# Kernel tuning notes

Measured on AMD Instinct MI355X. Metric: run time of the kernel, lower is better.

The kernel has to match this reference:

```python
import jax, jax.numpy as jnp
import numpy as np

N_TRIALS, T, INPUT_DIM = 32, 512, 64
N, R, OUTPUT_DIM = 4096, 8, 64
DT = 0.1


def setup_inputs() -> dict:
    key = jax.random.key(0)
    k_inp, k_B, k_W, k_m, k_n = jax.random.split(key, 5)
    inp = jax.random.normal(k_inp, (N_TRIALS, T, INPUT_DIM), dtype=jnp.float32)
    B = jax.random.normal(k_B, (N, INPUT_DIM), dtype=jnp.float32)
    W = jax.random.normal(k_W, (OUTPUT_DIM, N), dtype=jnp.float32) / np.sqrt(N)
    m = jax.random.normal(k_m, (N, R), dtype=jnp.float32)
    n = jax.random.normal(k_n, (N, R), dtype=jnp.float32)
    return {"inp": inp, "B": B, "W": W, "m": m, "n": n}


def reference(inp, B, W, m, n):
    # inp: [b, t, i]; B: [N, i]; W: [o, N]; m, n: [N, r]
    n_trials = inp.shape[0]
    # Precompute input projection for all steps: [t, b, N]
    inp_proj = jnp.einsum('bti,ni->tbn', inp, B)

    def step(x, u):
        # x: [b, N] voltage; u: [b, N] projected input at this step
        # sigmoid(x) @ (m n^T / N)^T == ((sigmoid(x) @ n) @ m^T) / N
        rec = (jax.nn.sigmoid(x) @ n) @ m.T / N
        x_new = (1.0 - DT) * x + DT * (rec + u)
        y = jax.nn.sigmoid(x_new) @ W.T  # [b, o]
        return x_new, (x_new, y)

    x0 = jnp.zeros((n_trials, N), dtype=inp.dtype)
    _, (xs, ys) = jax.lax.scan(step, x0, inp_proj)
    # xs: [t, b, N]; ys: [t, b, o]
    x_seq = jnp.concatenate([x0[None], xs], axis=0).transpose(1, 0, 2)  # [b, t+1, N]
    output_seq = ys.transpose(1, 0, 2)  # [b, t, o]
    return (x_seq, output_seq)
```

## Files before the change

### kernel.cpp

```cpp
#include <hip/hip_runtime.h>

static constexpr int BTRIALS = 32;
static constexpr int TSTEPS  = 512;
static constexpr int IDIM    = 64;
static constexpr int NDIM    = 4096;
static constexpr int RDIM    = 8;
static constexpr int ODIM    = 64;

__device__ __forceinline__ float fast_sigmoid(float x) {
    float e = __builtin_amdgcn_exp2f(x * -1.44269504088896340736f);
    return __builtin_amdgcn_rcpf(1.0f + e);
}

template <int CTRL, int RMASK>
__device__ __forceinline__ float dpp_add(float v) {
    int moved = __builtin_amdgcn_update_dpp(0, __float_as_int(v), CTRL, RMASK, 0xf, true);
    return v + __int_as_float(moved);
}

__device__ __forceinline__ float wave_reduce_to_lane63(float v) {
    v = dpp_add<0x111, 0xf>(v);
    v = dpp_add<0x112, 0xf>(v);
    v = dpp_add<0x114, 0xf>(v);
    v = dpp_add<0x118, 0xf>(v);
    v = dpp_add<0x142, 0xa>(v);
    v = dpp_add<0x143, 0xc>(v);
    return v;
}

__device__ __forceinline__ short f2bf(float f) {
    unsigned u = __float_as_uint(f);
    u += 0x7FFFu + ((u >> 16) & 1u);
    return (short)(u >> 16);
}

__global__ __launch_bounds__(256) void pre_gemm(const float* __restrict__ inp,
                                                const float* __restrict__ Bm,
                                                float* __restrict__ u,
                                                int t0, int rows) {
    __shared__ __align__(16) float At[64][68];
    __shared__ __align__(16) float Bt[64][68];
    const int tid = threadIdx.x;
    const int c4  = (tid & 15) * 4;
    const int rq  = tid >> 4;
    const int mbase = blockIdx.x * 64;
    const int nbase = blockIdx.y * 64;

    #pragma unroll
    for (int rr = 0; rr < 4; ++rr) {
        const int rloc = rr * 16 + rq;
        const int mr = mbase + rloc;
        float4 a = make_float4(0.f, 0.f, 0.f, 0.f);
        if (mr < rows) {
            const int b  = mr & 31;
            const int tl = mr >> 5;
            a = *(const float4*)(inp + ((size_t)b * TSTEPS + (t0 + tl)) * IDIM + c4);
        }
        At[c4 + 0][rloc] = a.x; At[c4 + 1][rloc] = a.y;
        At[c4 + 2][rloc] = a.z; At[c4 + 3][rloc] = a.w;
        const int n = nbase + rloc;
        float4 bb = *(const float4*)(Bm + (size_t)n * IDIM + c4);
        Bt[c4 + 0][rloc] = bb.x; Bt[c4 + 1][rloc] = bb.y;
        Bt[c4 + 2][rloc] = bb.z; Bt[c4 + 3][rloc] = bb.w;
    }
    __syncthreads();

    const int m4 = (tid >> 4) * 4;
    const int n4 = (tid & 15) * 4;
    float acc[4][4];
    #pragma unroll
    for (int i = 0; i < 4; ++i)
        #pragma unroll
        for (int j = 0; j < 4; ++j) acc[i][j] = 0.f;

    #pragma unroll 8
    for (int k = 0; k < 64; ++k) {
        float4 a = *(const float4*)&At[k][m4];
        float4 w = *(const float4*)&Bt[k][n4];
        float av[4] = {a.x, a.y, a.z, a.w};
        float wv[4] = {w.x, w.y, w.z, w.w};
        #pragma unroll
        for (int i = 0; i < 4; ++i)
            #pragma unroll
            for (int j = 0; j < 4; ++j)
                acc[i][j] = fmaf(av[i], wv[j], acc[i][j]);
    }

    #pragma unroll
    for (int i = 0; i < 4; ++i) {
        const int mr = mbase + m4 + i;
        if (mr < rows) {
            float4 o = make_float4(acc[i][0] * 0.1f, acc[i][1] * 0.1f,
                                   acc[i][2] * 0.1f, acc[i][3] * 0.1f);
            *(float4*)(u + (size_t)mr * NDIM + nbase + n4) = o;
        }
    }
}

__global__ __launch_bounds__(512, 2) void scan_kernel(const float* __restrict__ mmat,
                                                      const float* __restrict__ nmat,
                                                      const float* __restrict__ u,
                                                      float* __restrict__ xseq,
                                                      float* __restrict__ xstate,
                                                      int t0, int tc) {
    const int b    = blockIdx.x;
    const int tid  = threadIdx.x;
    const int j0   = tid * 8;
    const int lane = tid & 63;
    const int wv   = tid >> 6;

    __shared__ __align__(16) float wlds[2][64];

    float nm[8][8], mmr[8][8], x[8];
    const float4* np4 = (const float4*)(nmat + (size_t)j0 * RDIM);
    const float4* mp4 = (const float4*)(mmat + (size_t)j0 * RDIM);
    const float mscale = 0.1f / 4096.0f;
    #pragma unroll
    for (int j = 0; j < 8; ++j) {
        float4 a = np4[j * 2], c = np4[j * 2 + 1];
        nm[j][0] = a.x; nm[j][1] = a.y; nm[j][2] = a.z; nm[j][3] = a.w;
        nm[j][4] = c.x; nm[j][5] = c.y; nm[j][6] = c.z; nm[j][7] = c.w;
        float4 d = mp4[j * 2], e = mp4[j * 2 + 1];
        mmr[j][0] = d.x * mscale; mmr[j][1] = d.y * mscale;
        mmr[j][2] = d.z * mscale; mmr[j][3] = d.w * mscale;
        mmr[j][4] = e.x * mscale; mmr[j][5] = e.y * mscale;
        mmr[j][6] = e.z * mscale; mmr[j][7] = e.w * mscale;
    }

    if (t0 == 0) {
        #pragma unroll
        for (int j = 0; j < 8; ++j) x[j] = 0.0f;
        float* z = xseq + (size_t)b * (TSTEPS + 1) * NDIM + j0;
        *(float4*)(z + 0) = make_float4(0.f, 0.f, 0.f, 0.f);
        *(float4*)(z + 4) = make_float4(0.f, 0.f, 0.f, 0.f);
    } else {
        const float* xs = xstate + (size_t)b * NDIM + j0;
        float4 v0 = *(const float4*)(xs + 0);
        float4 v1 = *(const float4*)(xs + 4);
        x[0] = v0.x; x[1] = v0.y; x[2] = v0.z; x[3] = v0.w;
        x[4] = v1.x; x[5] = v1.y; x[6] = v1.z; x[7] = v1.w;
    }

    float uv[8];
    {
        const float* up = u + ((size_t)0 * BTRIALS + b) * NDIM + j0;
        float4 v0 = *(const float4*)(up + 0);
        float4 v1 = *(const float4*)(up + 4);
        uv[0] = v0.x; uv[1] = v0.y; uv[2] = v0.z; uv[3] = v0.w;
        uv[4] = v1.x; uv[5] = v1.y; uv[6] = v1.z; uv[7] = v1.w;
    }

    for (int tl = 0; tl < tc; ++tl) {
        const int buf = tl & 1;
        const int tn = (tl + 1 < tc) ? (tl + 1) : tl;
        const float* upn = u + ((size_t)tn * BTRIALS + b) * NDIM + j0;
        float4 pf0 = *(const float4*)(upn + 0);
        float4 pf1 = *(const float4*)(upn + 4);

        float part[8];
        #pragma unroll
        for (int r = 0; r < 8; ++r) part[r] = 0.0f;
        #pragma unroll
        for (int j = 0; j < 8; ++j) {
            float s = fast_sigmoid(x[j]);
            #pragma unroll
            for (int r = 0; r < 8; ++r) part[r] = fmaf(s, nm[j][r], part[r]);
        }
        #pragma unroll
        for (int r = 0; r < 8; ++r) part[r] = wave_reduce_to_lane63(part[r]);

        if (lane == 63) {
            #pragma unroll
            for (int r = 0; r < 8; ++r) wlds[buf][r * 8 + wv] = part[r];
        }

        float xd[8];
        #pragma unroll
        for (int j = 0; j < 8; ++j) xd[j] = fmaf(0.9f, x[j], uv[j]);

        __syncthreads();

        float v = wlds[buf][lane];
        v = dpp_add<0x111, 0xf>(v);
        v = dpp_add<0x112, 0xf>(v);
        v = dpp_add<0x114, 0xf>(v);

        float ps[8];
        #pragma unroll
        for (int r = 0; r < 8; ++r)
            ps[r] = __int_as_float(__builtin_amdgcn_readlane(__float_as_int(v), r * 8 + 7));

        float* xrow = xseq + ((size_t)b * (TSTEPS + 1) + (t0 + tl + 1)) * NDIM + j0;
        #pragma unroll
        for (int j = 0; j < 8; ++j) {
            float acc = xd[j];
            #pragma unroll
            for (int r = 0; r < 8; ++r) acc = fmaf(ps[r], mmr[j][r], acc);
            x[j] = acc;
        }
        *(float4*)(xrow + 0) = make_float4(x[0], x[1], x[2], x[3]);
        *(float4*)(xrow + 4) = make_float4(x[4], x[5], x[6], x[7]);

        uv[0] = pf0.x; uv[1] = pf0.y; uv[2] = pf0.z; uv[3] = pf0.w;
        uv[4] = pf1.x; uv[5] = pf1.y; uv[6] = pf1.z; uv[7] = pf1.w;
    }

    float* xs = xstate + (size_t)b * NDIM + j0;
    *(float4*)(xs + 0) = make_float4(x[0], x[1], x[2], x[3]);
    *(float4*)(xs + 4) = make_float4(x[4], x[5], x[6], x[7]);
}

typedef short v8s __attribute__((ext_vector_type(8)));
typedef float v4f __attribute__((ext_vector_type(4)));

__global__ __launch_bounds__(256) void y_gemm(const float* __restrict__ xseq,
                                              const float* __restrict__ Wm,
                                              float* __restrict__ yout) {
    const int tid  = threadIdx.x;
    const int lane = tid & 63;
    const int mt   = blockIdx.x * 4 + (tid >> 6);
    const int lm   = lane & 15;
    const int kq   = lane >> 4;

    const int m = mt * 16 + lm;
    const int g = m + (m >> 9) + 1;
    const float* pa = xseq + (size_t)g * NDIM + kq * 8;
    const float* pw = Wm + (size_t)lm * NDIM + kq * 8;

    v4f acc[4];
    #pragma unroll
    for (int ot = 0; ot < 4; ++ot) acc[ot] = (v4f){0.f, 0.f, 0.f, 0.f};

    for (int kc = 0; kc < NDIM; kc += 32) {
        float4 a0 = *(const float4*)(pa + kc);
        float4 a1 = *(const float4*)(pa + kc + 4);
        v8s af;
        af[0] = f2bf(fast_sigmoid(a0.x)); af[1] = f2bf(fast_sigmoid(a0.y));
        af[2] = f2bf(fast_sigmoid(a0.z)); af[3] = f2bf(fast_sigmoid(a0.w));
        af[4] = f2bf(fast_sigmoid(a1.x)); af[5] = f2bf(fast_sigmoid(a1.y));
        af[6] = f2bf(fast_sigmoid(a1.z)); af[7] = f2bf(fast_sigmoid(a1.w));
        #pragma unroll
        for (int ot = 0; ot < 4; ++ot) {
            const float* pwo = pw + (size_t)ot * 16 * NDIM + kc;
            float4 w0 = *(const float4*)(pwo);
            float4 w1 = *(const float4*)(pwo + 4);
            v8s bf;
            bf[0] = f2bf(w0.x); bf[1] = f2bf(w0.y);
            bf[2] = f2bf(w0.z); bf[3] = f2bf(w0.w);
            bf[4] = f2bf(w1.x); bf[5] = f2bf(w1.y);
            bf[6] = f2bf(w1.z); bf[7] = f2bf(w1.w);
            acc[ot] = __builtin_amdgcn_mfma_f32_16x16x32_bf16(af, bf, acc[ot], 0, 0, 0);
        }
    }

    #pragma unroll
    for (int ot = 0; ot < 4; ++ot) {
        #pragma unroll
        for (int r = 0; r < 4; ++r) {
            const int row = mt * 16 + kq * 4 + r;
            yout[(size_t)row * ODIM + ot * 16 + lm] = acc[ot][r];
        }
    }
}

extern "C" void kernel_launch(void* const* d_in, const int* in_sizes, int n_in,
                              void* d_out, int out_size, void* d_ws, size_t ws_size,
                              hipStream_t stream) {
    const float* inp = (const float*)d_in[0];
    const float* Bm  = (const float*)d_in[1];
    const float* Wm  = (const float*)d_in[2];
    const float* mm  = (const float*)d_in[3];
    const float* nm  = (const float*)d_in[4];

    float* out  = (float*)d_out;
    float* xseq = out;
    float* yout = out + (size_t)BTRIALS * (TSTEPS + 1) * NDIM;

    float* xstate = (float*)d_ws;
    float* ubuf   = xstate + (size_t)BTRIALS * NDIM;

    const size_t xbytes  = (size_t)BTRIALS * NDIM * sizeof(float);
    const size_t perstep = (size_t)BTRIALS * NDIM * sizeof(float);
    size_t avail = (ws_size > xbytes) ? (ws_size - xbytes) : 0;
    int Tc = (int)(avail / perstep);
    if (Tc > TSTEPS) Tc = TSTEPS;
    if (Tc < 1) Tc = 1;

    for (int t0 = 0; t0 < TSTEPS; t0 += Tc) {
        const int tc = (TSTEPS - t0 < Tc) ? (TSTEPS - t0) : Tc;
        const int rows = tc * BTRIALS;
        dim3 g1((rows + 63) / 64, NDIM / 64);
        pre_gemm<<<g1, 256, 0, stream>>>(inp, Bm, ubuf, t0, rows);
        scan_kernel<<<BTRIALS, 512, 0, stream>>>(mm, nm, ubuf, xseq, xstate, t0, tc);
    }
    y_gemm<<<(BTRIALS * TSTEPS) / 64, 256, 0, stream>>>(xseq, Wm, yout);
}
```

Baseline: 1.059 ms.

## Emit bf16 sigmoid states from scan and pre-convert W for the output GEMM

The scan kernel now computes sigmoid(x) once per step, reuses it for the next step's recurrence, and writes it as bf16 to a workspace buffer. The output GEMM reads these bf16 activations and a bf16 copy of W made by a new conversion kernel, instead of re-reading fp32 x and recomputing sigmoid and conversions. The y GEMM now runs per time chunk inside the loop. The scan kernel gains extra global writes, and the chunk size must be a multiple of 16 while each chunk needs more workspace.

```diff
diff --git a/kernel.cpp b/kernel.cpp
--- a/kernel.cpp
+++ b/kernel.cpp
@@ -6,6 +6,9 @@
 static constexpr int NDIM    = 4096;
 static constexpr int RDIM    = 8;
 static constexpr int ODIM    = 64;
+
+typedef short v8s __attribute__((ext_vector_type(8)));
+typedef float v4f __attribute__((ext_vector_type(4)));
 
 __device__ __forceinline__ float fast_sigmoid(float x) {
     float e = __builtin_amdgcn_exp2f(x * -1.44269504088896340736f);
@@ -97,11 +100,23 @@
     }
 }
 
+__global__ __launch_bounds__(256) void wconv(const float* __restrict__ W,
+                                             unsigned short* __restrict__ Wb) {
+    const int base = (blockIdx.x * 256 + threadIdx.x) * 8;
+    float4 a = *(const float4*)(W + base);
+    float4 b = *(const float4*)(W + base + 4);
+    v8s o;
+    o[0] = f2bf(a.x); o[1] = f2bf(a.y); o[2] = f2bf(a.z); o[3] = f2bf(a.w);
+    o[4] = f2bf(b.x); o[5] = f2bf(b.y); o[6] = f2bf(b.z); o[7] = f2bf(b.w);
+    *(v8s*)(Wb + base) = o;
+}
+
 __global__ __launch_bounds__(512, 2) void scan_kernel(const float* __restrict__ mmat,
                                                       const float* __restrict__ nmat,
                                                       const float* __restrict__ u,
                                                       float* __restrict__ xseq,
                                                       float* __restrict__ xstate,
+                                                      unsigned short* __restrict__ sbuf,
                                                       int t0, int tc) {
     const int b    = blockIdx.x;
     const int tid  = threadIdx.x;
@@ -111,7 +126,7 @@
 
     __shared__ __align__(16) float wlds[2][64];
 
-    float nm[8][8], mmr[8][8], x[8];
+    float nm[8][8], mmr[8][8], x[8], s[8];
     const float4* np4 = (const float4*)(nmat + (size_t)j0 * RDIM);
     const float4* mp4 = (const float4*)(mmat + (size_t)j0 * RDIM);
     const float mscale = 0.1f / 4096.0f;
@@ -140,6 +155,8 @@
         x[0] = v0.x; x[1] = v0.y; x[2] = v0.z; x[3] = v0.w;
         x[4] = v1.x; x[5] = v1.y; x[6] = v1.z; x[7] = v1.w;
     }
+    #pragma unroll
+    for (int j = 0; j < 8; ++j) s[j] = fast_sigmoid(x[j]);
 
     float uv[8];
     {
@@ -162,9 +179,8 @@
         for (int r = 0; r < 8; ++r) part[r] = 0.0f;
         #pragma unroll
         for (int j = 0; j < 8; ++j) {
-            float s = fast_sigmoid(x[j]);
             #pragma unroll
-            for (int r = 0; r < 8; ++r) part[r] = fmaf(s, nm[j][r], part[r]);
+            for (int r = 0; r < 8; ++r) part[r] = fmaf(s[j], nm[j][r], part[r]);
         }
         #pragma unroll
         for (int r = 0; r < 8; ++r) part[r] = wave_reduce_to_lane63(part[r]);
@@ -201,6 +217,13 @@
         *(float4*)(xrow + 0) = make_float4(x[0], x[1], x[2], x[3]);
         *(float4*)(xrow + 4) = make_float4(x[4], x[5], x[6], x[7]);
 
+        #pragma unroll
+        for (int j = 0; j < 8; ++j) s[j] = fast_sigmoid(x[j]);
+        v8s sv;
+        sv[0] = f2bf(s[0]); sv[1] = f2bf(s[1]); sv[2] = f2bf(s[2]); sv[3] = f2bf(s[3]);
+        sv[4] = f2bf(s[4]); sv[5] = f2bf(s[5]); sv[6] = f2bf(s[6]); sv[7] = f2bf(s[7]);
+        *(v8s*)(sbuf + ((size_t)b * tc + tl) * NDIM + j0) = sv;
+
         uv[0] = pf0.x; uv[1] = pf0.y; uv[2] = pf0.z; uv[3] = pf0.w;
         uv[4] = pf1.x; uv[5] = pf1.y; uv[6] = pf1.z; uv[7] = pf1.w;
     }
@@ -210,45 +233,33 @@
     *(float4*)(xs + 4) = make_float4(x[4], x[5], x[6], x[7]);
 }
 
-typedef short v8s __attribute__((ext_vector_type(8)));
-typedef float v4f __attribute__((ext_vector_type(4)));
-
-__global__ __launch_bounds__(256) void y_gemm(const float* __restrict__ xseq,
-                                              const float* __restrict__ Wm,
-                                              float* __restrict__ yout) {
+__global__ __launch_bounds__(256) void y_gemm(const unsigned short* __restrict__ sbuf,
+                                              const unsigned short* __restrict__ Wb,
+                                              float* __restrict__ yout,
+                                              int t0, int tc) {
     const int tid  = threadIdx.x;
     const int lane = tid & 63;
     const int mt   = blockIdx.x * 4 + (tid >> 6);
     const int lm   = lane & 15;
     const int kq   = lane >> 4;
 
-    const int m = mt * 16 + lm;
-    const int g = m + (m >> 9) + 1;
-    const float* pa = xseq + (size_t)g * NDIM + kq * 8;
-    const float* pw = Wm + (size_t)lm * NDIM + kq * 8;
+    const int tilesPerB = tc >> 4;
+    const int b  = mt / tilesPerB;
+    const int tt = mt % tilesPerB;
+
+    const unsigned short* pa = sbuf + ((size_t)b * tc + tt * 16 + lm) * NDIM + kq * 8;
+    const unsigned short* pw = Wb + (size_t)lm * NDIM + kq * 8;
 
     v4f acc[4];
     #pragma unroll
     for (int ot = 0; ot < 4; ++ot) acc[ot] = (v4f){0.f, 0.f, 0.f, 0.f};
 
+    #pragma unroll 4
     for (int kc = 0; kc < NDIM; kc += 32) {
-        float4 a0 = *(const float4*)(pa + kc);
-        float4 a1 = *(const float4*)(pa + kc + 4);
-        v8s af;
-        af[0] = f2bf(fast_sigmoid(a0.x)); af[1] = f2bf(fast_sigmoid(a0.y));
-        af[2] = f2bf(fast_sigmoid(a0.z)); af[3] = f2bf(fast_sigmoid(a0.w));
-        af[4] = f2bf(fast_sigmoid(a1.x)); af[5] = f2bf(fast_sigmoid(a1.y));
-        af[6] = f2bf(fast_sigmoid(a1.z)); af[7] = f2bf(fast_sigmoid(a1.w));
+        v8s af = *(const v8s*)(pa + kc);
         #pragma unroll
         for (int ot = 0; ot < 4; ++ot) {
-            const float* pwo = pw + (size_t)ot * 16 * NDIM + kc;
-            float4 w0 = *(const float4*)(pwo);
-            float4 w1 = *(const float4*)(pwo + 4);
-            v8s bf;
-            bf[0] = f2bf(w0.x); bf[1] = f2bf(w0.y);
-            bf[2] = f2bf(w0.z); bf[3] = f2bf(w0.w);
-            bf[4] = f2bf(w1.x); bf[5] = f2bf(w1.y);
-            bf[6] = f2bf(w1.z); bf[7] = f2bf(w1.w);
+            v8s bf = *(const v8s*)(pw + (size_t)ot * 16 * NDIM + kc);
             acc[ot] = __builtin_amdgcn_mfma_f32_16x16x32_bf16(af, bf, acc[ot], 0, 0, 0);
         }
     }
@@ -257,7 +268,7 @@
     for (int ot = 0; ot < 4; ++ot) {
         #pragma unroll
         for (int r = 0; r < 4; ++r) {
-            const int row = mt * 16 + kq * 4 + r;
+            const int row = b * TSTEPS + t0 + tt * 16 + kq * 4 + r;
             yout[(size_t)row * ODIM + ot * 16 + lm] = acc[ot][r];
         }
     }
@@ -277,21 +288,28 @@
     float* yout = out + (size_t)BTRIALS * (TSTEPS + 1) * NDIM;
 
     float* xstate = (float*)d_ws;
-    float* ubuf   = xstate + (size_t)BTRIALS * NDIM;
-
-    const size_t xbytes  = (size_t)BTRIALS * NDIM * sizeof(float);
-    const size_t perstep = (size_t)BTRIALS * NDIM * sizeof(float);
-    size_t avail = (ws_size > xbytes) ? (ws_size - xbytes) : 0;
+    unsigned short* Wb = (unsigned short*)(xstate + (size_t)BTRIALS * NDIM);
+    const size_t head = (size_t)BTRIALS * NDIM * sizeof(float)
+                      + (size_t)ODIM * NDIM * sizeof(unsigned short);
+    float* ubuf = (float*)((char*)d_ws + head);
+
+    const size_t perstep = (size_t)BTRIALS * NDIM * (sizeof(float) + sizeof(unsigned short));
+    size_t avail = (ws_size > head) ? (ws_size - head) : 0;
     int Tc = (int)(avail / perstep);
     if (Tc > TSTEPS) Tc = TSTEPS;
-    if (Tc < 1) Tc = 1;
+    Tc &= ~15;
+    if (Tc < 16) Tc = 16;
+
+    wconv<<<(ODIM * NDIM) / (256 * 8), 256, 0, stream>>>(Wm, Wb);
 
     for (int t0 = 0; t0 < TSTEPS; t0 += Tc) {
         const int tc = (TSTEPS - t0 < Tc) ? (TSTEPS - t0) : Tc;
+        unsigned short* sbuf = (unsigned short*)(ubuf + (size_t)tc * BTRIALS * NDIM);
         const int rows = tc * BTRIALS;
         dim3 g1((rows + 63) / 64, NDIM / 64);
         pre_gemm<<<g1, 256, 0, stream>>>(inp, Bm, ubuf, t0, rows);
-        scan_kernel<<<BTRIALS, 512, 0, stream>>>(mm, nm, ubuf, xseq, xstate, t0, tc);
-    }
-    y_gemm<<<(BTRIALS * TSTEPS) / 64, 256, 0, stream>>>(xseq, Wm, yout);
-}
+        scan_kernel<<<BTRIALS, 512, 0, stream>>>(mm, nm, ubuf, xseq, xstate, sbuf, t0, tc);
+        const int mtiles = BTRIALS * (tc / 16);
+        y_gemm<<<mtiles / 4, 256, 0, stream>>>(sbuf, Wb, yout, t0, tc);
+    }
+}
```

Result: no change. 1.060 ms (+0.1%).
